# Performance work log

Hardware: AMD Instinct MI355X
Metric: run time of the kernel (lower is better)

The kernel has to match this reference:

```python
import jax, jax.numpy as jnp
import numpy as np

EPS = 1e-10


def setup_inputs() -> dict:
    key = jax.random.key(0)
    k1, k2, k3 = jax.random.split(key, 3)
    B, N, S = 2, 16384, 4096
    return {
        "xyz": jax.random.normal(k1, (B, 3, N), dtype=jnp.float32),
        "sparse_xyz": jax.random.normal(k2, (B, 3, S), dtype=jnp.float32),
        "sparse_flow": jax.random.normal(k3, (B, 3, S), dtype=jnp.float32),
    }


def reference(xyz, sparse_xyz, sparse_flow):
    # channel-last views: x [B,N,3], s [B,S,3], f [B,S,3]
    x = jnp.transpose(xyz, (0, 2, 1))
    s = jnp.transpose(sparse_xyz, (0, 2, 1))
    f = jnp.transpose(sparse_flow, (0, 2, 1))

    # squared pairwise distances [B,N,S] (knn_point / square_distance)
    d2 = (
        jnp.sum(x * x, axis=-1)[:, :, None]
        + jnp.sum(s * s, axis=-1)[:, None, :]
        - 2.0 * jnp.einsum("bnc,bsc->bns", x, s)
    )
    # 3 nearest sparse neighbors of each dense point
    _, knn_idx = jax.lax.top_k(-d2, 3)  # [B,N,3]

    # index_points_group: gather neighbor coords/flows per batch
    gather = jax.vmap(lambda tbl, idx: tbl[idx])  # ([S,3],[N,3]) -> [N,3,3]
    grouped_xyz = gather(s, knn_idx)              # [B,N,3,3]
    grouped_flow = gather(f, knn_idx)             # [B,N,3,3]

    # inverse-distance weights (Euclidean dist, clamped)
    diff = grouped_xyz - x[:, :, None, :]
    dist = jnp.maximum(jnp.linalg.norm(diff, axis=3), EPS)  # [B,N,3]
    inv = 1.0 / dist
    weight = inv / jnp.sum(inv, axis=2, keepdims=True)      # [B,N,3]

    dense_flow = jnp.sum(weight[..., None] * grouped_flow, axis=2)  # [B,N,3]
    return jnp.transpose(dense_flow, (0, 2, 1))  # [B,3,N]
```

## Files before the change

### kernel.cpp

```cpp
#include <hip/hip_runtime.h>


constexpr int S_SPARSE = 4096;
constexpr int NSPLIT   = 32;
constexpr int Q        = 8;
constexpr int THREADS  = 256;
constexpr int PPB      = THREADS * Q / NSPLIT;
constexpr int NITER    = S_SPARSE / NSPLIT;
constexpr int K        = 4;
constexpr int KM       = 8;
constexpr int KROW     = NSPLIT * K + 4;
constexpr int KBUF2_OFF = PPB * KROW * 4;

__device__ __forceinline__ unsigned med3u(unsigned a, unsigned b, unsigned c) {
    unsigned d;
    asm("v_med3_u32 %0, %1, %2, %3" : "=v"(d) : "v"(a), "v"(b), "v"(c));
    return d;
}

__global__ __launch_bounds__(THREADS)
void upsample_knn3(const float* __restrict__ xyz,
                   const float* __restrict__ sxyz,
                   const float* __restrict__ sflow,
                   float* __restrict__ out,
                   int N)
{
    __shared__ __align__(16) unsigned char smem_raw[S_SPARSE * sizeof(float4)];
    float4*   sp    = reinterpret_cast<float4*>(smem_raw);
    unsigned* kbuf  = reinterpret_cast<unsigned*>(smem_raw);
    uint4*    kbuf2 = reinterpret_cast<uint4*>(smem_raw + KBUF2_OFF);

    const int b = blockIdx.y;
    const int t = threadIdx.x;
    const int g = t >> 5;
    const int s = t & 31;

    const float* sx = sxyz + (size_t)b * 3 * S_SPARSE;
    const float* sy = sx + S_SPARSE;
    const float* sz = sy + S_SPARSE;
    #pragma unroll
    for (int it = 0; it < S_SPARSE / (THREADS * 4); ++it) {
        const int j0 = (t + it * THREADS) * 4;
        const float4 vx = *reinterpret_cast<const float4*>(sx + j0);
        const float4 vy = *reinterpret_cast<const float4*>(sy + j0);
        const float4 vz = *reinterpret_cast<const float4*>(sz + j0);
        sp[j0 + 0] = make_float4(vx.x, vy.x, vz.x, 0.0f);
        sp[j0 + 1] = make_float4(vx.y, vy.y, vz.y, 0.0f);
        sp[j0 + 2] = make_float4(vx.z, vy.z, vz.z, 0.0f);
        sp[j0 + 3] = make_float4(vx.w, vy.w, vz.w, 0.0f);
    }

    const float* xb = xyz + (size_t)b * 3 * N;
    const int p0 = blockIdx.x * PPB + g * Q;
    float qx[Q], qy[Q], qz[Q];
    {
        const float4 x0 = *reinterpret_cast<const float4*>(xb + p0);
        const float4 x1 = *reinterpret_cast<const float4*>(xb + p0 + 4);
        const float4 y0 = *reinterpret_cast<const float4*>(xb + N + p0);
        const float4 y1 = *reinterpret_cast<const float4*>(xb + N + p0 + 4);
        const float4 z0 = *reinterpret_cast<const float4*>(xb + 2 * N + p0);
        const float4 z1 = *reinterpret_cast<const float4*>(xb + 2 * N + p0 + 4);
        qx[0]=x0.x; qx[1]=x0.y; qx[2]=x0.z; qx[3]=x0.w; qx[4]=x1.x; qx[5]=x1.y; qx[6]=x1.z; qx[7]=x1.w;
        qy[0]=y0.x; qy[1]=y0.y; qy[2]=y0.z; qy[3]=y0.w; qy[4]=y1.x; qy[5]=y1.y; qy[6]=y1.z; qy[7]=y1.w;
        qz[0]=z0.x; qz[1]=z0.y; qz[2]=z0.z; qz[3]=z0.w; qz[4]=z1.x; qz[5]=z1.y; qz[6]=z1.z; qz[7]=z1.w;
    }
    __syncthreads();

    unsigned k0[Q], k1[Q], k2[Q], k3[Q];
    #pragma unroll
    for (int q = 0; q < Q; ++q) { k0[q]=0xFFFFFFFFu; k1[q]=0xFFFFFFFFu; k2[q]=0xFFFFFFFFu; k3[q]=0xFFFFFFFFu; }

    #pragma unroll 2
    for (int i = 0; i < NITER; ++i) {
        const int    j = (i << 5) | s;
        const float4 p = sp[j];
        #pragma unroll
        for (int q = 0; q < Q; ++q) {
            const float dx = qx[q] - p.x;
            const float dy = qy[q] - p.y;
            const float dz = qz[q] - p.z;
            const float d2 = dx * dx + dy * dy + dz * dz;
            const unsigned c = (__float_as_uint(d2) & 0xFFFFF000u) | (unsigned)j;
            k3[q] = med3u(k2[q], k3[q], c);
            k2[q] = med3u(k1[q], k2[q], c);
            k1[q] = med3u(k0[q], k1[q], c);
            k0[q] = min(k0[q], c);
        }
    }

    __syncthreads();
    #pragma unroll
    for (int q = 0; q < Q; ++q) {
        const int lp = g * Q + q;
        *reinterpret_cast<uint4*>(&kbuf[lp * KROW + s * K]) =
            make_uint4(k0[q], k1[q], k2[q], k3[q]);
    }
    __syncthreads();

    {
        const int lp = t >> 2;
        const int qd = t & 3;
        unsigned m0 = 0xFFFFFFFFu, m1 = 0xFFFFFFFFu, m2 = 0xFFFFFFFFu, m3 = 0xFFFFFFFFu;
        const unsigned* rowp = kbuf + lp * KROW + qd * 32;
        #pragma unroll
        for (int c = 0; c < 32; c += 4) {
            const uint4 v = *reinterpret_cast<const uint4*>(rowp + c);
            #pragma unroll
            for (int e = 0; e < 4; ++e) {
                const unsigned cc = (&v.x)[e];
                m3 = med3u(m2, m3, cc);
                m2 = med3u(m1, m2, cc);
                m1 = med3u(m0, m1, cc);
                m0 = min(m0, cc);
            }
        }
        kbuf2[lp * 4 + qd] = make_uint4(m0, m1, m2, m3);
    }
    __syncthreads();

    if (t < PPB) {
        unsigned bk[KM];
        #pragma unroll
        for (int k = 0; k < KM; ++k) bk[k] = 0xFFFFFFFFu;
        #pragma unroll
        for (int c4 = 0; c4 < 4; ++c4) {
            const uint4 v = kbuf2[t * 4 + c4];
            #pragma unroll
            for (int e = 0; e < 4; ++e) {
                const unsigned cc = (&v.x)[e];
                bk[7] = med3u(bk[6], bk[7], cc);
                bk[6] = med3u(bk[5], bk[6], cc);
                bk[5] = med3u(bk[4], bk[5], cc);
                bk[4] = med3u(bk[3], bk[4], cc);
                bk[3] = med3u(bk[2], bk[3], cc);
                bk[2] = med3u(bk[1], bk[2], cc);
                bk[1] = med3u(bk[0], bk[1], cc);
                bk[0] = min(bk[0], cc);
            }
        }

        const int pt = blockIdx.x * PPB + t;
        const double qxd = (double)xb[pt];
        const double qyd = (double)xb[N + pt];
        const double qzd = (double)xb[2 * N + pt];

        double e0 = 1e300, e1 = 1e300, e2 = 1e300;
        int    j0 = 0,     j1 = 0,     j2 = 0;
        #pragma unroll
        for (int c = 0; c < KM; ++c) {
            const int    j  = (int)(bk[c] & 0xFFFu);
            const double dx = qxd - (double)sx[j];
            const double dy = qyd - (double)sy[j];
            const double dz = qzd - (double)sz[j];
            const double d2 = dx * dx + dy * dy + dz * dz;
            if (d2 < e2) {
                if (d2 < e1) {
                    e2 = e1; j2 = j1;
                    if (d2 < e0) { e1 = e0; j1 = j0; e0 = d2; j0 = j; }
                    else         { e1 = d2; j1 = j; }
                } else {
                    e2 = d2; j2 = j;
                }
            }
        }

        double dist0 = sqrt(e0); dist0 = dist0 > 1e-10 ? dist0 : 1e-10;
        double dist1 = sqrt(e1); dist1 = dist1 > 1e-10 ? dist1 : 1e-10;
        double dist2 = sqrt(e2); dist2 = dist2 > 1e-10 ? dist2 : 1e-10;
        const double inv0 = 1.0 / dist0;
        const double inv1 = 1.0 / dist1;
        const double inv2 = 1.0 / dist2;
        const double wsum = inv0 + inv1 + inv2;

        const float* fb = sflow + (size_t)b * 3 * S_SPARSE;
        float*       ob = out   + (size_t)b * 3 * N;
        #pragma unroll
        for (int c = 0; c < 3; ++c) {
            const float* fc = fb + c * S_SPARSE;
            const double o =
                (inv0 * (double)fc[j0] +
                 inv1 * (double)fc[j1] +
                 inv2 * (double)fc[j2]) / wsum;
            ob[c * N + pt] = (float)o;
        }
    }
}

extern "C" void kernel_launch(void* const* d_in, const int* in_sizes, int n_in,
                              void* d_out, int out_size, void* d_ws, size_t ws_size,
                              hipStream_t stream)
{
    const float* xyz  = (const float*)d_in[0];
    const float* sxyz = (const float*)d_in[1];
    const float* sflw = (const float*)d_in[2];
    float*       out  = (float*)d_out;

    const int B = 2;
    const int N = in_sizes[0] / (3 * B);

    dim3 grid(N / PPB, B);
    upsample_knn3<<<grid, THREADS, 0, stream>>>(xyz, sxyz, sflw, out, N);
}
```

Before: 47.80 us.

## Split sparse scan across 64 lanes, keep top-3 per lane, prefetch SoA LDS loads

Doubles the split of the sparse set so each of the 64 lanes in a wavefront owns a slice of sparse points and each block handles 32 query points instead of 64. Each lane now keeps only 3 candidates per query instead of 4, which removes one med3 per distance. Sparse coordinates are copied into LDS as three planar arrays, and the next point is prefetched one iteration ahead. The two-level candidate merge is reworked to combine 8 chunks of 24 into top-5 lists before the final top-8 and fp64 refinement. The cost is fewer queries per block, which means more blocks each reloading the whole sparse set, plus more scalar LDS traffic. Keeping fewer candidates per lane also slightly raises the chance that a true neighbour is lost before the exact refinement.

```diff
diff --git a/kernel.cpp b/kernel.cpp
--- a/kernel.cpp
+++ b/kernel.cpp
@@ -2,15 +2,17 @@
 
 
 constexpr int S_SPARSE = 4096;
-constexpr int NSPLIT   = 32;
+constexpr int NSPLIT   = 64;
 constexpr int Q        = 8;
 constexpr int THREADS  = 256;
 constexpr int PPB      = THREADS * Q / NSPLIT;
 constexpr int NITER    = S_SPARSE / NSPLIT;
-constexpr int K        = 4;
+constexpr int K        = 3;
+constexpr int KA       = 5;
 constexpr int KM       = 8;
-constexpr int KROW     = NSPLIT * K + 4;
-constexpr int KBUF2_OFF = PPB * KROW * 4;
+constexpr int KROW     = NSPLIT * K + 8;
+constexpr int KBUF2_OFF_DW = PPB * KROW;
+constexpr int SLIN_PAD = 64;
 
 __device__ __forceinline__ unsigned med3u(unsigned a, unsigned b, unsigned c) {
     unsigned d;
@@ -25,29 +27,23 @@
                    float* __restrict__ out,
                    int N)
 {
-    __shared__ __align__(16) unsigned char smem_raw[S_SPARSE * sizeof(float4)];
-    float4*   sp    = reinterpret_cast<float4*>(smem_raw);
-    unsigned* kbuf  = reinterpret_cast<unsigned*>(smem_raw);
-    uint4*    kbuf2 = reinterpret_cast<uint4*>(smem_raw + KBUF2_OFF);
+    __shared__ __align__(16) unsigned char smem_raw[(3 * S_SPARSE + SLIN_PAD) * 4];
+    float*    slin = reinterpret_cast<float*>(smem_raw);
+    unsigned* kbuf = reinterpret_cast<unsigned*>(smem_raw);
 
     const int b = blockIdx.y;
     const int t = threadIdx.x;
-    const int g = t >> 5;
-    const int s = t & 31;
+    const int g = t >> 6;
+    const int s = t & 63;
 
     const float* sx = sxyz + (size_t)b * 3 * S_SPARSE;
     const float* sy = sx + S_SPARSE;
     const float* sz = sy + S_SPARSE;
     #pragma unroll
-    for (int it = 0; it < S_SPARSE / (THREADS * 4); ++it) {
+    for (int it = 0; it < 3 * S_SPARSE / (THREADS * 4); ++it) {
         const int j0 = (t + it * THREADS) * 4;
-        const float4 vx = *reinterpret_cast<const float4*>(sx + j0);
-        const float4 vy = *reinterpret_cast<const float4*>(sy + j0);
-        const float4 vz = *reinterpret_cast<const float4*>(sz + j0);
-        sp[j0 + 0] = make_float4(vx.x, vy.x, vz.x, 0.0f);
-        sp[j0 + 1] = make_float4(vx.y, vy.y, vz.y, 0.0f);
-        sp[j0 + 2] = make_float4(vx.z, vy.z, vz.z, 0.0f);
-        sp[j0 + 3] = make_float4(vx.w, vy.w, vz.w, 0.0f);
+        *reinterpret_cast<float4*>(slin + j0) =
+            *reinterpret_cast<const float4*>(sx + j0);
     }
 
     const float* xb = xyz + (size_t)b * 3 * N;
@@ -66,22 +62,27 @@
     }
     __syncthreads();
 
-    unsigned k0[Q], k1[Q], k2[Q], k3[Q];
+    unsigned k0[Q], k1[Q], k2[Q];
     #pragma unroll
-    for (int q = 0; q < Q; ++q) { k0[q]=0xFFFFFFFFu; k1[q]=0xFFFFFFFFu; k2[q]=0xFFFFFFFFu; k3[q]=0xFFFFFFFFu; }
-
-    #pragma unroll 2
+    for (int q = 0; q < Q; ++q) { k0[q]=0xFFFFFFFFu; k1[q]=0xFFFFFFFFu; k2[q]=0xFFFFFFFFu; }
+
+    float px = slin[s], py = slin[s + S_SPARSE], pz = slin[s + 2 * S_SPARSE];
+
+    #pragma unroll 4
     for (int i = 0; i < NITER; ++i) {
-        const int    j = (i << 5) | s;
-        const float4 p = sp[j];
+        const float cx = px, cy = py, cz = pz;
+        const int   cj = (i << 6) | s;
+        const int   jn = cj + 64;
+        px = slin[jn];
+        py = slin[jn + S_SPARSE];
+        pz = slin[jn + 2 * S_SPARSE];
         #pragma unroll
         for (int q = 0; q < Q; ++q) {
-            const float dx = qx[q] - p.x;
-            const float dy = qy[q] - p.y;
-            const float dz = qz[q] - p.z;
+            const float dx = qx[q] - cx;
+            const float dy = qy[q] - cy;
+            const float dz = qz[q] - cz;
             const float d2 = dx * dx + dy * dy + dz * dz;
-            const unsigned c = (__float_as_uint(d2) & 0xFFFFF000u) | (unsigned)j;
-            k3[q] = med3u(k2[q], k3[q], c);
+            const unsigned c = (__float_as_uint(d2) & 0xFFFFF000u) | (unsigned)cj;
             k2[q] = med3u(k1[q], k2[q], c);
             k1[q] = med3u(k0[q], k1[q], c);
             k0[q] = min(k0[q], c);
@@ -91,30 +92,29 @@
     __syncthreads();
     #pragma unroll
     for (int q = 0; q < Q; ++q) {
-        const int lp = g * Q + q;
-        *reinterpret_cast<uint4*>(&kbuf[lp * KROW + s * K]) =
-            make_uint4(k0[q], k1[q], k2[q], k3[q]);
+        const int base = (g * Q + q) * KROW + s * K;
+        kbuf[base + 0] = k0[q];
+        kbuf[base + 1] = k1[q];
+        kbuf[base + 2] = k2[q];
     }
     __syncthreads();
 
     {
-        const int lp = t >> 2;
-        const int qd = t & 3;
-        unsigned m0 = 0xFFFFFFFFu, m1 = 0xFFFFFFFFu, m2 = 0xFFFFFFFFu, m3 = 0xFFFFFFFFu;
-        const unsigned* rowp = kbuf + lp * KROW + qd * 32;
-        #pragma unroll
-        for (int c = 0; c < 32; c += 4) {
-            const uint4 v = *reinterpret_cast<const uint4*>(rowp + c);
-            #pragma unroll
-            for (int e = 0; e < 4; ++e) {
-                const unsigned cc = (&v.x)[e];
-                m3 = med3u(m2, m3, cc);
-                m2 = med3u(m1, m2, cc);
-                m1 = med3u(m0, m1, cc);
-                m0 = min(m0, cc);
-            }
-        }
-        kbuf2[lp * 4 + qd] = make_uint4(m0, m1, m2, m3);
+        const int lp = t >> 3;
+        const int ch = t & 7;
+        unsigned m0=0xFFFFFFFFu, m1=0xFFFFFFFFu, m2=0xFFFFFFFFu, m3=0xFFFFFFFFu, m4=0xFFFFFFFFu;
+        const unsigned* rowp = kbuf + lp * KROW + ch * 24;
+        #pragma unroll
+        for (int c = 0; c < 24; ++c) {
+            const unsigned cc = rowp[c];
+            m4 = med3u(m3, m4, cc);
+            m3 = med3u(m2, m3, cc);
+            m2 = med3u(m1, m2, cc);
+            m1 = med3u(m0, m1, cc);
+            m0 = min(m0, cc);
+        }
+        unsigned* o = kbuf + KBUF2_OFF_DW + (lp * 8 + ch) * KA;
+        o[0]=m0; o[1]=m1; o[2]=m2; o[3]=m3; o[4]=m4;
     }
     __syncthreads();
 
@@ -122,21 +122,18 @@
         unsigned bk[KM];
         #pragma unroll
         for (int k = 0; k < KM; ++k) bk[k] = 0xFFFFFFFFu;
-        #pragma unroll
-        for (int c4 = 0; c4 < 4; ++c4) {
-            const uint4 v = kbuf2[t * 4 + c4];
-            #pragma unroll
-            for (int e = 0; e < 4; ++e) {
-                const unsigned cc = (&v.x)[e];
-                bk[7] = med3u(bk[6], bk[7], cc);
-                bk[6] = med3u(bk[5], bk[6], cc);
-                bk[5] = med3u(bk[4], bk[5], cc);
-                bk[4] = med3u(bk[3], bk[4], cc);
-                bk[3] = med3u(bk[2], bk[3], cc);
-                bk[2] = med3u(bk[1], bk[2], cc);
-                bk[1] = med3u(bk[0], bk[1], cc);
-                bk[0] = min(bk[0], cc);
-            }
+        const unsigned* inp = kbuf + KBUF2_OFF_DW + t * 8 * KA;
+        #pragma unroll
+        for (int c = 0; c < 8 * KA; ++c) {
+            const unsigned cc = inp[c];
+            bk[7] = med3u(bk[6], bk[7], cc);
+            bk[6] = med3u(bk[5], bk[6], cc);
+            bk[5] = med3u(bk[4], bk[5], cc);
+            bk[4] = med3u(bk[3], bk[4], cc);
+            bk[3] = med3u(bk[2], bk[3], cc);
+            bk[2] = med3u(bk[1], bk[2], cc);
+            bk[1] = med3u(bk[0], bk[1], cc);
+            bk[0] = min(bk[0], cc);
         }
 
         const int pt = blockIdx.x * PPB + t;
```

After: 44.22 us. -7.5%, faster.
